# Optimization experiments

Measured on AMD Instinct MI355X. Metric: run time of the kernel, lower is better.

The kernel has to match this reference:

```python
import jax, jax.numpy as jnp
import numpy as np
from jax import lax

SIZE = 4096
NUM_CONVS = 5
FC_IN = 16 * 16
EPS = 1e-5


def _forward(x_real, x_imag, mag_kernel, phase_kernel, conv_w, conv_b,
             bn_gamma, bn_beta, bn_mean, bn_var, prelu_a,
             fc5_w, fc5_b, ln_gamma, ln_beta, prelu5_a, fc6_w, fc6_b):
    # KernelModule51: magnitude/phase scaling -> recombine -> ifftshift -> ifft2 -> real
    mag = jnp.sqrt(x_real * x_real + x_imag * x_imag) * mag_kernel      # (1,S,S)
    ph = jnp.arctan2(x_imag, x_real) * phase_kernel                     # (1,S,S)
    combined = lax.complex(mag * jnp.cos(ph), mag * jnp.sin(ph))        # m*exp(i*p)
    x = jnp.fft.ifft2(jnp.fft.ifftshift(combined, axes=(-2, -1)), axes=(-2, -1)).real
    x = x[:, None, :, :]  # (1,1,S,S) NCHW

    for i in range(NUM_CONVS):
        x = lax.conv_general_dilated(x, conv_w[i], window_strides=(3, 3), padding='VALID',
                                     dimension_numbers=('NCHW', 'OIHW', 'NCHW'))
        x = x + conv_b[i][None, :, None, None]
        scale = (bn_gamma[i] * lax.rsqrt(bn_var[i] + EPS))[None, :, None, None]
        shift = (bn_beta[i] - bn_gamma[i] * bn_mean[i] * lax.rsqrt(bn_var[i] + EPS))[None, :, None, None]
        x = x * scale + shift
        x = jnp.where(x >= 0, x, prelu_a[i] * x)

    x = x.reshape(x.shape[0], -1)                                       # (1, FC_IN)
    x = x @ fc5_w + fc5_b                                               # (1, 82)
    mu = jnp.mean(x, axis=-1, keepdims=True)
    var = jnp.mean((x - mu) ** 2, axis=-1, keepdims=True)
    x = (x - mu) * lax.rsqrt(var + EPS) * ln_gamma + ln_beta
    x = jnp.where(x >= 0, x, prelu5_a * x)
    return x @ fc6_w + fc6_b                                            # (1, 5)


def setup_inputs() -> dict:
    key = jax.random.key(0)
    ks = jax.random.split(key, 9)
    f32 = jnp.float32
    return {
        'x_real': jax.random.normal(ks[0], (1, SIZE, SIZE), f32),
        'x_imag': jax.random.normal(ks[1], (1, SIZE, SIZE), f32),
        'mag_kernel': jax.random.normal(ks[2], (1, SIZE, SIZE), f32),
        'phase_kernel': jax.random.normal(ks[3], (1, SIZE, SIZE), f32),
        'conv_w': jax.random.normal(ks[4], (NUM_CONVS, 1, 1, 3, 3), f32) * 0.33,
        'conv_b': jax.random.normal(ks[5], (NUM_CONVS, 1), f32) * 0.1,
        'bn_gamma': jnp.ones((NUM_CONVS, 1), f32),
        'bn_beta': jnp.zeros((NUM_CONVS, 1), f32),
        'bn_mean': jnp.zeros((NUM_CONVS, 1), f32),
        'bn_var': jnp.ones((NUM_CONVS, 1), f32),
        'prelu_a': jnp.full((NUM_CONVS,), 0.25, f32),
        'fc5_w': jax.random.normal(ks[6], (FC_IN, 82), f32) * (1.0 / np.sqrt(FC_IN)),
        'fc5_b': jnp.zeros((82,), f32),
        'ln_gamma': jnp.ones((82,), f32),
        'ln_beta': jnp.zeros((82,), f32),
        'prelu5_a': jnp.asarray(0.25, f32),
        'fc6_w': jax.random.normal(ks[7], (82, 5), f32) * (1.0 / np.sqrt(82.0)),
        'fc6_b': jnp.zeros((5,), f32),
    }


def reference(x_real, x_imag, mag_kernel, phase_kernel, conv_w, conv_b,
              bn_gamma, bn_beta, bn_mean, bn_var, prelu_a,
              fc5_w, fc5_b, ln_gamma, ln_beta, prelu5_a, fc6_w, fc6_b):
    return _forward(x_real, x_imag, mag_kernel, phase_kernel, conv_w, conv_b,
                    bn_gamma, bn_beta, bn_mean, bn_var, prelu_a,
                    fc5_w, fc5_b, ln_gamma, ln_beta, prelu5_a, fc6_w, fc6_b)
```

## Files before the change

kernel.cpp:

```cpp
#include <hip/hip_runtime.h>
#include <math.h>

#define N 4096
#define TPB 256
#define PI2_F 6.283185307179586f
#define PAD(i) ((i) + ((i) >> 4))

__device__ __forceinline__ float2 cmul(float2 a, float2 b) {
    return make_float2(a.x * b.x - a.y * b.y, a.x * b.y + a.y * b.x);
}
__device__ __forceinline__ float2 cadd(float2 a, float2 b) { return make_float2(a.x + b.x, a.y + b.y); }
__device__ __forceinline__ float2 csub(float2 a, float2 b) { return make_float2(a.x - b.x, a.y - b.y); }
__device__ __forceinline__ float2 muli(float2 a) { return make_float2(-a.y, a.x); }

__device__ __forceinline__ void ifft16(float2 v[16]) {
    const float C1 = 0.9238795325112867f, S1 = 0.3826834323650898f;
    const float C2 = 0.7071067811865476f;
    float2 y[16];
    #pragma unroll
    for (int t = 0; t < 4; ++t) {
        float2 a0 = v[t], a1 = v[t + 4], a2 = v[t + 8], a3 = v[t + 12];
        float2 t0 = cadd(a0, a2), t1 = csub(a0, a2);
        float2 t2 = cadd(a1, a3), t3 = muli(csub(a1, a3));
        float2 c0 = cadd(t0, t2), c1 = cadd(t1, t3);
        float2 c2 = csub(t0, t2), c3 = csub(t1, t3);
        if (t == 0) {
            y[0] = c0; y[1] = c1; y[2] = c2; y[3] = c3;
        } else if (t == 1) {
            y[4] = c0;
            y[5] = cmul(c1, make_float2(C1, S1));
            y[6] = cmul(c2, make_float2(C2, C2));
            y[7] = cmul(c3, make_float2(S1, C1));
        } else if (t == 2) {
            y[8] = c0;
            y[9]  = cmul(c1, make_float2(C2, C2));
            y[10] = muli(c2);
            y[11] = cmul(c3, make_float2(-C2, C2));
        } else {
            y[12] = c0;
            y[13] = cmul(c1, make_float2(S1, C1));
            y[14] = cmul(c2, make_float2(-C2, C2));
            y[15] = cmul(c3, make_float2(-C1, -S1));
        }
    }
    #pragma unroll
    for (int t = 0; t < 4; ++t) {
        float2 a0 = y[t], a1 = y[t + 4], a2 = y[t + 8], a3 = y[t + 12];
        float2 t0 = cadd(a0, a2), t1 = csub(a0, a2);
        float2 t2 = cadd(a1, a3), t3 = muli(csub(a1, a3));
        v[t]      = cadd(t0, t2);
        v[t + 4]  = cadd(t1, t3);
        v[t + 8]  = csub(t0, t2);
        v[t + 12] = csub(t1, t3);
    }
}

__global__ __launch_bounds__(TPB, 4) void k_fft_rows_fused(
    const float* __restrict__ xr, const float* __restrict__ xi,
    const float* __restrict__ mk, const float* __restrict__ pk,
    float2* __restrict__ out)
{
    __shared__ float2 lds[4096 + 256];
    const int t = threadIdx.x;
    const size_t base = (size_t)blockIdx.x * N;
    float2 v[16];

    #pragma unroll
    for (int q = 0; q < 16; ++q) {
        int idx = t + 256 * q;
        float a = xr[base + idx];
        float b = xi[base + idx];
        float mag = sqrtf(a * a + b * b) * mk[base + idx];
        float ph  = atan2f(b, a) * pk[base + idx];
        float s, c;
        sincosf(ph, &s, &c);
        v[q] = make_float2(mag * c, mag * s);
    }

    ifft16(v);
    {
        float s1, c1;
        __sincosf(PI2_F * (float)t * (1.0f / 4096.0f), &s1, &c1);
        float2 w1 = make_float2(c1, s1);
        float2 w = make_float2(1.0f, 0.0f);
        #pragma unroll
        for (int p = 0; p < 16; ++p) {
            lds[PAD(16 * t + p)] = cmul(v[p], w);
            w = cmul(w, w1);
        }
    }
    __syncthreads();
    #pragma unroll
    for (int q = 0; q < 16; ++q) v[q] = lds[PAD(t + 256 * q)];
    __syncthreads();

    ifft16(v);
    {
        int j = t >> 4, k = t & 15;
        float s1, c1;
        __sincosf(PI2_F * (float)j * (1.0f / 256.0f), &s1, &c1);
        float2 w1 = make_float2(c1, s1);
        float2 w = make_float2(1.0f, 0.0f);
        int dbase = j * 256 + k;
        #pragma unroll
        for (int p = 0; p < 16; ++p) {
            lds[PAD(dbase + 16 * p)] = cmul(v[p], w);
            w = cmul(w, w1);
        }
    }
    __syncthreads();
    #pragma unroll
    for (int q = 0; q < 16; ++q) v[q] = lds[PAD(t + 256 * q)];

    ifft16(v);
    #pragma unroll
    for (int p = 0; p < 16; ++p) out[base + t + 256 * p] = v[p];
}

__global__ void k_transpose(const float2* __restrict__ in,
                            float2* __restrict__ out)
{
    __shared__ float2 tile[32][33];
    const int bx = blockIdx.x * 32, by = blockIdx.y * 32;
    const int tx = threadIdx.x, ty = threadIdx.y;
    #pragma unroll
    for (int k = 0; k < 4; ++k)
        tile[ty + k * 8][tx] = in[(size_t)(by + ty + k * 8) * N + bx + tx];
    __syncthreads();
    #pragma unroll
    for (int k = 0; k < 4; ++k)
        out[(size_t)(bx + ty + k * 8) * N + by + tx] = tile[tx][ty + k * 8];
}

__global__ __launch_bounds__(TPB, 4) void k_fft_rows_final(
    const float2* __restrict__ in, float* __restrict__ out)
{
    __shared__ float2 lds[4096 + 256];
    const int t = threadIdx.x;
    const int row = blockIdx.x;
    const size_t base = (size_t)row * N;
    float2 v[16];

    #pragma unroll
    for (int q = 0; q < 16; ++q) v[q] = in[base + t + 256 * q];

    ifft16(v);
    {
        float s1, c1;
        __sincosf(PI2_F * (float)t * (1.0f / 4096.0f), &s1, &c1);
        float2 w1 = make_float2(c1, s1);
        float2 w = make_float2(1.0f, 0.0f);
        #pragma unroll
        for (int p = 0; p < 16; ++p) {
            lds[PAD(16 * t + p)] = cmul(v[p], w);
            w = cmul(w, w1);
        }
    }
    __syncthreads();
    #pragma unroll
    for (int q = 0; q < 16; ++q) v[q] = lds[PAD(t + 256 * q)];
    __syncthreads();

    ifft16(v);
    {
        int j = t >> 4, k = t & 15;
        float s1, c1;
        __sincosf(PI2_F * (float)j * (1.0f / 256.0f), &s1, &c1);
        float2 w1 = make_float2(c1, s1);
        float2 w = make_float2(1.0f, 0.0f);
        int dbase = j * 256 + k;
        #pragma unroll
        for (int p = 0; p < 16; ++p) {
            lds[PAD(dbase + 16 * p)] = cmul(v[p], w);
            w = cmul(w, w1);
        }
    }
    __syncthreads();
    #pragma unroll
    for (int q = 0; q < 16; ++q) v[q] = lds[PAD(t + 256 * q)];

    ifft16(v);

    const float scale = 1.0f / 16777216.0f;
    const float sgn = ((row + t) & 1) ? -scale : scale;
    #pragma unroll
    for (int p = 0; p < 16; ++p) out[base + t + 256 * p] = v[p].x * sgn;
}

__global__ void k_conv(const float* __restrict__ in, float* __restrict__ out,
                       int win, int wout,
                       const float* __restrict__ cw, const float* __restrict__ cb,
                       const float* __restrict__ bg, const float* __restrict__ bb,
                       const float* __restrict__ bm, const float* __restrict__ bv,
                       const float* __restrict__ pa, int layer)
{
    int idx = blockIdx.x * blockDim.x + threadIdx.x;
    if (idx >= wout * wout) return;
    int r = idx / wout, c = idx % wout;
    const float* w = cw + layer * 9;
    float acc = 0.0f;
    #pragma unroll
    for (int di = 0; di < 3; ++di)
        #pragma unroll
        for (int dj = 0; dj < 3; ++dj)
            acc += in[(size_t)(3 * r + dj) * win + (3 * c + di)] * w[di * 3 + dj];
    float g  = bg[layer];
    float rs = rsqrtf(bv[layer] + 1e-5f);
    float scale = g * rs;
    float shift = bb[layer] - g * bm[layer] * rs;
    float v = (acc + cb[layer]) * scale + shift;
    float a = pa[layer];
    out[idx] = v >= 0.0f ? v : a * v;
}

__global__ __launch_bounds__(256) void k_head(
    const float* __restrict__ xt,
    const float* __restrict__ w5, const float* __restrict__ b5,
    const float* __restrict__ lg, const float* __restrict__ lb,
    const float* __restrict__ p5a,
    const float* __restrict__ w6, const float* __restrict__ b6,
    float* __restrict__ out)
{
    __shared__ float sx[256];
    __shared__ float h[82];
    __shared__ float red[2];
    const int tid = threadIdx.x;
    int m = tid >> 4, n = tid & 15;
    sx[tid] = xt[n * 16 + m];
    __syncthreads();
    if (tid < 82) {
        float acc = b5[tid];
        for (int k = 0; k < 256; ++k) acc += sx[k] * w5[k * 82 + tid];
        h[tid] = acc;
    }
    __syncthreads();
    if (tid == 0) {
        float mu = 0.0f;
        for (int o = 0; o < 82; ++o) mu += h[o];
        mu *= (1.0f / 82.0f);
        float var = 0.0f;
        for (int o = 0; o < 82; ++o) { float d = h[o] - mu; var += d * d; }
        var *= (1.0f / 82.0f);
        red[0] = mu;
        red[1] = rsqrtf(var + 1e-5f);
    }
    __syncthreads();
    if (tid < 82) {
        float v = (h[tid] - red[0]) * red[1] * lg[tid] + lb[tid];
        float a = p5a[0];
        h[tid] = v >= 0.0f ? v : a * v;
    }
    __syncthreads();
    if (tid < 5) {
        float acc = b6[tid];
        for (int o = 0; o < 82; ++o) acc += h[o] * w6[o * 5 + tid];
        out[tid] = acc;
    }
}

extern "C" void kernel_launch(void* const* d_in, const int* in_sizes, int n_in,
                              void* d_out, int out_size, void* d_ws, size_t ws_size,
                              hipStream_t stream)
{
    const float* xr  = (const float*)d_in[0];
    const float* xi  = (const float*)d_in[1];
    const float* mk  = (const float*)d_in[2];
    const float* pk  = (const float*)d_in[3];
    const float* cw  = (const float*)d_in[4];
    const float* cb  = (const float*)d_in[5];
    const float* bg  = (const float*)d_in[6];
    const float* bb  = (const float*)d_in[7];
    const float* bm  = (const float*)d_in[8];
    const float* bv  = (const float*)d_in[9];
    const float* pa  = (const float*)d_in[10];
    const float* w5  = (const float*)d_in[11];
    const float* b5  = (const float*)d_in[12];
    const float* lg  = (const float*)d_in[13];
    const float* lb  = (const float*)d_in[14];
    const float* p5a = (const float*)d_in[15];
    const float* w6  = (const float*)d_in[16];
    const float* b6  = (const float*)d_in[17];
    float* outp = (float*)d_out;

    char* ws = (char*)d_ws;
    const size_t HALF = (size_t)128 * 1024 * 1024;
    float2* A = (float2*)ws;
    float2* B = (float2*)(ws + HALF);
    float*  ximg = (float*)ws;
    float* c1 = (float*)(ws + HALF);
    float* c2 = c1 + 1365 * 1365;
    float* c3 = c2 + 455 * 455;
    float* c4 = c3 + 151 * 151;
    float* c5 = c4 + 50 * 50;

    k_fft_rows_fused<<<N, TPB, 0, stream>>>(xr, xi, mk, pk, A);
    k_transpose<<<dim3(N / 32, N / 32), dim3(32, 8), 0, stream>>>(A, B);
    k_fft_rows_final<<<N, TPB, 0, stream>>>(B, ximg);

    k_conv<<<(1365 * 1365 + 255) / 256, 256, 0, stream>>>(ximg, c1, 4096, 1365,
        cw, cb, bg, bb, bm, bv, pa, 0);
    k_conv<<<(455 * 455 + 255) / 256, 256, 0, stream>>>(c1, c2, 1365, 455,
        cw, cb, bg, bb, bm, bv, pa, 1);
    k_conv<<<(151 * 151 + 255) / 256, 256, 0, stream>>>(c2, c3, 455, 151,
        cw, cb, bg, bb, bm, bv, pa, 2);
    k_conv<<<(50 * 50 + 255) / 256, 256, 0, stream>>>(c3, c4, 151, 50,
        cw, cb, bg, bb, bm, bv, pa, 3);
    k_conv<<<(16 * 16 + 255) / 256, 256, 0, stream>>>(c4, c5, 50, 16,
        cw, cb, bg, bb, bm, bv, pa, 4);

    k_head<<<1, 256, 0, stream>>>(c5, w5, b5, lg, lb, p5a, w6, b6, outp);
}
```

Before: 442.3 us.

## Store FFT intermediate in fp16, use fast atan2/sincos, fuse conv tail into head

The intermediate spectrum between the row FFT, the transpose and the column FFT is now stored as half2, with a 1/4096 prescale to avoid overflow. This halves the traffic of the transpose and intermediate buffers. atan2f and sincosf are replaced by a polynomial approximation and the hardware intrinsic. The last two conv layers are fused with the FC/LayerNorm head into a single-block kernel, removing two launches. The cost is reduced precision from fp16 storage and the approximate transcendentals, which may break tolerance.

```diff
diff --git a/kernel.cpp b/kernel.cpp
--- a/kernel.cpp
+++ b/kernel.cpp
@@ -1,4 +1,5 @@
 #include <hip/hip_runtime.h>
+#include <hip/hip_fp16.h>
 #include <math.h>
 
 #define N 4096
@@ -12,6 +13,18 @@
 __device__ __forceinline__ float2 cadd(float2 a, float2 b) { return make_float2(a.x + b.x, a.y + b.y); }
 __device__ __forceinline__ float2 csub(float2 a, float2 b) { return make_float2(a.x - b.x, a.y - b.y); }
 __device__ __forceinline__ float2 muli(float2 a) { return make_float2(-a.y, a.x); }
+
+__device__ __forceinline__ float fast_atan2f(float y, float x) {
+    float ax = fabsf(x), ay = fabsf(y);
+    float mx = fmaxf(ax, ay), mn = fminf(ax, ay);
+    float t = mn * __builtin_amdgcn_rcpf(fmaxf(mx, 1e-37f));
+    float s = t * t;
+    float r = fmaf(s, fmaf(s, fmaf(s, fmaf(s, 0.0208351f, -0.0851330f),
+                                    0.1801410f), -0.3302995f), 0.9998660f) * t;
+    if (ay > ax) r = 1.5707963267948966f - r;
+    if (x < 0.0f) r = 3.1415926535897932f - r;
+    return copysignf(r, y);
+}
 
 __device__ __forceinline__ void ifft16(float2 v[16]) {
     const float C1 = 0.9238795325112867f, S1 = 0.3826834323650898f;
@@ -58,7 +71,7 @@
 __global__ __launch_bounds__(TPB, 4) void k_fft_rows_fused(
     const float* __restrict__ xr, const float* __restrict__ xi,
     const float* __restrict__ mk, const float* __restrict__ pk,
-    float2* __restrict__ out)
+    __half2* __restrict__ out)
 {
     __shared__ float2 lds[4096 + 256];
     const int t = threadIdx.x;
@@ -71,9 +84,9 @@
         float a = xr[base + idx];
         float b = xi[base + idx];
         float mag = sqrtf(a * a + b * b) * mk[base + idx];
-        float ph  = atan2f(b, a) * pk[base + idx];
+        float ph  = fast_atan2f(b, a) * pk[base + idx];
         float s, c;
-        sincosf(ph, &s, &c);
+        __sincosf(ph, &s, &c);
         v[q] = make_float2(mag * c, mag * s);
     }
 
@@ -113,14 +126,16 @@
     for (int q = 0; q < 16; ++q) v[q] = lds[PAD(t + 256 * q)];
 
     ifft16(v);
-    #pragma unroll
-    for (int p = 0; p < 16; ++p) out[base + t + 256 * p] = v[p];
-}
-
-__global__ void k_transpose(const float2* __restrict__ in,
-                            float2* __restrict__ out)
-{
-    __shared__ float2 tile[32][33];
+    const float S = 1.0f / 4096.0f;
+    #pragma unroll
+    for (int p = 0; p < 16; ++p)
+        out[base + t + 256 * p] = __floats2half2_rn(v[p].x * S, v[p].y * S);
+}
+
+__global__ void k_transpose(const unsigned int* __restrict__ in,
+                            unsigned int* __restrict__ out)
+{
+    __shared__ unsigned int tile[32][33];
     const int bx = blockIdx.x * 32, by = blockIdx.y * 32;
     const int tx = threadIdx.x, ty = threadIdx.y;
     #pragma unroll
@@ -133,7 +148,7 @@
 }
 
 __global__ __launch_bounds__(TPB, 4) void k_fft_rows_final(
-    const float2* __restrict__ in, float* __restrict__ out)
+    const __half2* __restrict__ in, float* __restrict__ out)
 {
     __shared__ float2 lds[4096 + 256];
     const int t = threadIdx.x;
@@ -142,7 +157,7 @@
     float2 v[16];
 
     #pragma unroll
-    for (int q = 0; q < 16; ++q) v[q] = in[base + t + 256 * q];
+    for (int q = 0; q < 16; ++q) v[q] = __half22float2(in[base + t + 256 * q]);
 
     ifft16(v);
     {
@@ -181,22 +196,19 @@
 
     ifft16(v);
 
-    const float scale = 1.0f / 16777216.0f;
+    const float scale = 1.0f / 4096.0f;
     const float sgn = ((row + t) & 1) ? -scale : scale;
     #pragma unroll
     for (int p = 0; p < 16; ++p) out[base + t + 256 * p] = v[p].x * sgn;
 }
 
-__global__ void k_conv(const float* __restrict__ in, float* __restrict__ out,
-                       int win, int wout,
-                       const float* __restrict__ cw, const float* __restrict__ cb,
-                       const float* __restrict__ bg, const float* __restrict__ bb,
-                       const float* __restrict__ bm, const float* __restrict__ bv,
-                       const float* __restrict__ pa, int layer)
-{
-    int idx = blockIdx.x * blockDim.x + threadIdx.x;
-    if (idx >= wout * wout) return;
-    int r = idx / wout, c = idx % wout;
+__device__ __forceinline__ float conv_bn_prelu(
+    const float* __restrict__ in, int win, int r, int c,
+    const float* __restrict__ cw, const float* __restrict__ cb,
+    const float* __restrict__ bg, const float* __restrict__ bb,
+    const float* __restrict__ bm, const float* __restrict__ bv,
+    const float* __restrict__ pa, int layer)
+{
     const float* w = cw + layer * 9;
     float acc = 0.0f;
     #pragma unroll
@@ -210,24 +222,70 @@
     float shift = bb[layer] - g * bm[layer] * rs;
     float v = (acc + cb[layer]) * scale + shift;
     float a = pa[layer];
-    out[idx] = v >= 0.0f ? v : a * v;
-}
-
-__global__ __launch_bounds__(256) void k_head(
-    const float* __restrict__ xt,
+    return v >= 0.0f ? v : a * v;
+}
+
+__global__ void k_conv(const float* __restrict__ in, float* __restrict__ out,
+                       int win, int wout,
+                       const float* __restrict__ cw, const float* __restrict__ cb,
+                       const float* __restrict__ bg, const float* __restrict__ bb,
+                       const float* __restrict__ bm, const float* __restrict__ bv,
+                       const float* __restrict__ pa, int layer)
+{
+    int idx = blockIdx.x * blockDim.x + threadIdx.x;
+    if (idx >= wout * wout) return;
+    int r = idx / wout, c = idx % wout;
+    out[idx] = conv_bn_prelu(in, win, r, c, cw, cb, bg, bb, bm, bv, pa, layer);
+}
+
+__global__ __launch_bounds__(1024) void k_tail(
+    const float* __restrict__ c3img,
+    const float* __restrict__ cw, const float* __restrict__ cb,
+    const float* __restrict__ bg, const float* __restrict__ bb,
+    const float* __restrict__ bm, const float* __restrict__ bv,
+    const float* __restrict__ pa,
     const float* __restrict__ w5, const float* __restrict__ b5,
     const float* __restrict__ lg, const float* __restrict__ lb,
     const float* __restrict__ p5a,
     const float* __restrict__ w6, const float* __restrict__ b6,
     float* __restrict__ out)
 {
+    __shared__ float s4[2500];
+    __shared__ float s5[256];
     __shared__ float sx[256];
     __shared__ float h[82];
     __shared__ float red[2];
     const int tid = threadIdx.x;
-    int m = tid >> 4, n = tid & 15;
-    sx[tid] = xt[n * 16 + m];
-    __syncthreads();
+
+    for (int idx = tid; idx < 2500; idx += 1024) {
+        int r = idx / 50, c = idx % 50;
+        s4[idx] = conv_bn_prelu(c3img, 151, r, c, cw, cb, bg, bb, bm, bv, pa, 3);
+    }
+    __syncthreads();
+
+    if (tid < 256) {
+        int r = tid >> 4, c = tid & 15;
+        const float* w = cw + 4 * 9;
+        float acc = 0.0f;
+        #pragma unroll
+        for (int di = 0; di < 3; ++di)
+            #pragma unroll
+            for (int dj = 0; dj < 3; ++dj)
+                acc += s4[(3 * r + dj) * 50 + (3 * c + di)] * w[di * 3 + dj];
+        float g  = bg[4];
+        float rs = rsqrtf(bv[4] + 1e-5f);
+        float v = (acc + cb[4]) * (g * rs) + (bb[4] - g * bm[4] * rs);
+        float a = pa[4];
+        s5[tid] = v >= 0.0f ? v : a * v;
+    }
+    __syncthreads();
+
+    if (tid < 256) {
+        int m = tid >> 4, n = tid & 15;
+        sx[tid] = s5[n * 16 + m];
+    }
+    __syncthreads();
+
     if (tid < 82) {
         float acc = b5[tid];
         for (int k = 0; k < 256; ++k) acc += sx[k] * w5[k * 82 + tid];
@@ -283,18 +341,17 @@
     float* outp = (float*)d_out;
 
     char* ws = (char*)d_ws;
-    const size_t HALF = (size_t)128 * 1024 * 1024;
-    float2* A = (float2*)ws;
-    float2* B = (float2*)(ws + HALF);
-    float*  ximg = (float*)ws;
-    float* c1 = (float*)(ws + HALF);
+    const size_t Q = (size_t)64 * 1024 * 1024;
+    __half2* A = (__half2*)ws;
+    __half2* B = (__half2*)(ws + Q);
+    float*  ximg = (float*)(ws + 2 * Q);
+    float* c1 = (float*)ws;
     float* c2 = c1 + 1365 * 1365;
     float* c3 = c2 + 455 * 455;
-    float* c4 = c3 + 151 * 151;
-    float* c5 = c4 + 50 * 50;
 
     k_fft_rows_fused<<<N, TPB, 0, stream>>>(xr, xi, mk, pk, A);
-    k_transpose<<<dim3(N / 32, N / 32), dim3(32, 8), 0, stream>>>(A, B);
+    k_transpose<<<dim3(N / 32, N / 32), dim3(32, 8), 0, stream>>>(
+        (const unsigned int*)A, (unsigned int*)B);
     k_fft_rows_final<<<N, TPB, 0, stream>>>(B, ximg);
 
     k_conv<<<(1365 * 1365 + 255) / 256, 256, 0, stream>>>(ximg, c1, 4096, 1365,
@@ -303,10 +360,7 @@
         cw, cb, bg, bb, bm, bv, pa, 1);
     k_conv<<<(151 * 151 + 255) / 256, 256, 0, stream>>>(c2, c3, 455, 151,
         cw, cb, bg, bb, bm, bv, pa, 2);
-    k_conv<<<(50 * 50 + 255) / 256, 256, 0, stream>>>(c3, c4, 151, 50,
-        cw, cb, bg, bb, bm, bv, pa, 3);
-    k_conv<<<(16 * 16 + 255) / 256, 256, 0, stream>>>(c4, c5, 50, 16,
-        cw, cb, bg, bb, bm, bv, pa, 4);
-
-    k_head<<<1, 256, 0, stream>>>(c5, w5, b5, lg, lb, p5a, w6, b6, outp);
-}
+
+    k_tail<<<1, 1024, 0, stream>>>(c3, cw, cb, bg, bb, bm, bv, pa,
+                                   w5, b5, lg, lb, p5a, w6, b6, outp);
+}
```

New measurement: 378.4 us. -14.4%, faster.
